# Kernel tuning notes

Measured on AMD Instinct MI355X. Metric: run time of the kernel, lower is better.

The kernel has to match this reference:

```python
import jax, jax.numpy as jnp
import numpy as np

D_MODEL = 4096
NUM_EXPERTS = 64
TOP_K = 2


def setup_inputs() -> dict:
    key = jax.random.key(0)
    kx, kw, kb = jax.random.split(key, 3)
    x = jax.random.normal(kx, (4, 4096, D_MODEL), dtype=jnp.float32)
    # nn.Linear(d_model, num_experts): weight [E, D], bias [E]
    bound = 1.0 / np.sqrt(D_MODEL)
    W = jax.random.uniform(kw, (NUM_EXPERTS, D_MODEL), dtype=jnp.float32, minval=-bound, maxval=bound)
    b = jax.random.uniform(kb, (NUM_EXPERTS,), dtype=jnp.float32, minval=-bound, maxval=bound)
    return {"x": x, "W": W, "b": b}


def reference(x, W, b):
    # logits = gate(x): [B, S, E]
    logits = jnp.einsum("bsd,ed->bse", x, W) + b
    scores = jax.nn.softmax(logits, axis=-1)
    topk_scores, topk_idx = jax.lax.top_k(scores, TOP_K)  # [B,S,K]
    # scatter top-k scores back into a dense [B,S,E] dispatch mask
    onehot = jax.nn.one_hot(topk_idx, NUM_EXPERTS, dtype=scores.dtype)  # [B,S,K,E]
    dispatch_mask = jnp.einsum("bske,bsk->bse", onehot, topk_scores)
    return dispatch_mask
```

## Files before the change

kernel.cpp:

```cpp
#include <hip/hip_runtime.h>
#include <hip/hip_bf16.h>
#include <math.h>
#include <stdint.h>

#define DM 4096
#define NEXP 64
#define BK 64
#define NCH (DM / BK)
#define TOKPB 16

typedef short bf16x8 __attribute__((ext_vector_type(8)));
typedef float f32x4  __attribute__((ext_vector_type(4)));

#define SMEM_BYTES 8192

__device__ __forceinline__ void split2(float f0, float f1, uint32_t& hw, uint32_t& lw) {
    float2 ff; ff.x = f0; ff.y = f1;
    __hip_bfloat162 h = __float22bfloat162_rn(ff);
    union { __hip_bfloat162 b; uint32_t u; } ch; ch.b = h;
    hw = ch.u;
    float h0 = __bfloat162float(h.x);
    float h1 = __bfloat162float(h.y);
    float2 gg; gg.x = f0 - h0; gg.y = f1 - h1;
    __hip_bfloat162 l = __float22bfloat162_rn(gg);
    union { __hip_bfloat162 b; uint32_t u; } cl; cl.b = l;
    lw = cl.u;
}

__global__ __launch_bounds__(512) void wsplit_kernel(const float* __restrict__ W,
                                                     char* __restrict__ blob) {
    const int c   = blockIdx.x;
    const int tid = threadIdx.x;
    const int e   = tid >> 3;
    const int g   = tid & 7;

    const float* src = W + (size_t)e * DM + c * BK + g * 8;
    float x[8];
    *(float4*)(x)     = *(const float4*)(src);
    *(float4*)(x + 4) = *(const float4*)(src + 4);

    uint32_t hiw[4], low[4];
#pragma unroll
    for (int j = 0; j < 4; ++j) split2(x[2 * j], x[2 * j + 1], hiw[j], low[j]);

    const int ks = g >> 2;
    const int ln = (e & 15) | ((g & 3) << 4);
    const int n4 = e >> 4;
    const size_t base = (size_t)c * 16384 + (size_t)ks * 4096 + (size_t)n4 * 1024 + (size_t)ln * 16;
    *(uint4*)(blob + base)        = *(uint4*)hiw;
    *(uint4*)(blob + base + 8192) = *(uint4*)low;
}

__global__ __launch_bounds__(128) void router_mfma_kernel(
    const float* __restrict__ X,
    const char* __restrict__ blob,
    const float* __restrict__ Bv,
    float* __restrict__ out)
{
    __shared__ __align__(16) char smem[SMEM_BYTES];

    const int tid  = threadIdx.x;
    const int lane = tid & 63;
    const int wv   = tid >> 6;
    const long tok0 = (long)blockIdx.x * TOKPB;

    const int tkn = tid >> 3;
    const int kq  = tid & 7;
    const size_t rowbase = (size_t)(tok0 + tkn) * DM + kq * 8;

    f32x4 acc[2];
    acc[0] = (f32x4)0.0f;
    acc[1] = (f32x4)0.0f;

    float xa[8], xb[8];

    auto loadX = [&](float* xr, int c) {
        const float* p = X + rowbase + c * BK;
        *(float4*)(xr)     = *(const float4*)(p);
        *(float4*)(xr + 4) = *(const float4*)(p + 4);
    };

    auto cvtWrite = [&](const float* xr, int buf) {
        uint32_t hw[4], lw[4];
#pragma unroll
        for (int j = 0; j < 4; ++j) split2(xr[2 * j], xr[2 * j + 1], hw[j], lw[j]);
        const int slot = (kq ^ (tkn & 7)) * 16;
        char* bh = smem + ((buf * 2 + 0) * TOKPB + tkn) * 128;
        char* bl = smem + ((buf * 2 + 1) * TOKPB + tkn) * 128;
        *(uint4*)(bh + slot) = *(uint4*)hw;
        *(uint4*)(bl + slot) = *(uint4*)lw;
    };

    const int tk = lane & 15;
    const int kg = lane >> 4;
    const int sw = tk & 7;

    auto compute = [&](int buf, int c) {
        const char* bb = blob + (size_t)c * 16384;
#pragma unroll
        for (int ks = 0; ks < 2; ++ks) {
            const int gA   = ks * 4 + kg;
            const int slot = (gA ^ sw) * 16;
            bf16x8 ah = *(const bf16x8*)(smem + ((buf * 2 + 0) * TOKPB + tk) * 128 + slot);
            bf16x8 al = *(const bf16x8*)(smem + ((buf * 2 + 1) * TOKPB + tk) * 128 + slot);
#pragma unroll
            for (int n = 0; n < 2; ++n) {
                const int n4 = wv * 2 + n;
                const size_t bo = (size_t)ks * 4096 + (size_t)n4 * 1024 + (size_t)lane * 16;
                bf16x8 bh = *(const bf16x8*)(bb + bo);
                bf16x8 bl = *(const bf16x8*)(bb + 8192 + bo);
                acc[n] = __builtin_amdgcn_mfma_f32_16x16x32_bf16(ah, bh, acc[n], 0, 0, 0);
                acc[n] = __builtin_amdgcn_mfma_f32_16x16x32_bf16(ah, bl, acc[n], 0, 0, 0);
                acc[n] = __builtin_amdgcn_mfma_f32_16x16x32_bf16(al, bh, acc[n], 0, 0, 0);
                acc[n] = __builtin_amdgcn_mfma_f32_16x16x32_bf16(al, bl, acc[n], 0, 0, 0);
            }
        }
    };

    loadX(xa, 0);
    cvtWrite(xa, 0);
    __syncthreads();

#pragma unroll 1
    for (int cc = 0; cc < NCH / 2; ++cc) {
        const int c0 = 2 * cc;
        loadX(xb, c0 + 1);
        compute(0, c0);
        cvtWrite(xb, 1);
        __syncthreads();
        if (cc + 1 < NCH / 2) {
            loadX(xa, c0 + 2);
            compute(1, c0 + 1);
            cvtWrite(xa, 0);
        } else {
            compute(1, c0 + 1);
        }
        __syncthreads();
    }

#pragma unroll
    for (int n = 0; n < 2; ++n) {
        const int ee = (wv * 2 + n) * 16 + tk;
#pragma unroll
        for (int r = 0; r < 4; ++r) {
            const int tl = kg * 4 + r;
            *(float*)(smem + tl * 264 + ee * 4) = acc[n][r];
        }
    }
    __syncthreads();

    const float bias = Bv[lane];
#pragma unroll 1
    for (int j = 0; j < 8; ++j) {
        const int t = wv * 8 + j;
        float v = *(const float*)(smem + t * 264 + lane * 4) + bias;

        float m1 = v;        int i1 = lane;
        float m2 = -3.4e38f; int i2 = 127;
#pragma unroll
        for (int s = 1; s < 64; s <<= 1) {
            float om1 = __shfl_xor(m1, s, 64);
            int   oi1 = __shfl_xor(i1, s, 64);
            float om2 = __shfl_xor(m2, s, 64);
            int   oi2 = __shfl_xor(i2, s, 64);
            bool bw = (om1 > m1) || (om1 == m1 && oi1 < i1);
            float l1v = bw ? m1 : om1;  int l1i = bw ? i1 : oi1;
            float w2v = bw ? om2 : m2;  int w2i = bw ? oi2 : i2;
            if (bw) { m1 = om1; i1 = oi1; }
            bool tw = (l1v > w2v) || (l1v == w2v && l1i < w2i);
            m2 = tw ? l1v : w2v;  i2 = tw ? l1i : w2i;
        }

        float p = expf(v - m1);
        float ssum = p;
#pragma unroll
        for (int s = 1; s < 64; s <<= 1) ssum += __shfl_xor(ssum, s, 64);

        float sc = (lane == i1 || lane == i2) ? (p / ssum) : 0.0f;
        out[(size_t)(tok0 + t) * NEXP + lane] = sc;
    }
}

extern "C" void kernel_launch(void* const* d_in, const int* in_sizes, int n_in,
                              void* d_out, int out_size, void* d_ws, size_t ws_size,
                              hipStream_t stream) {
    const float* X  = (const float*)d_in[0];
    const float* W  = (const float*)d_in[1];
    const float* Bv = (const float*)d_in[2];
    float* out = (float*)d_out;

    char* blob = (char*)d_ws;
    wsplit_kernel<<<dim3(NCH), dim3(512), 0, stream>>>(W, blob);

    const int n_tokens = 4 * 4096;
    router_mfma_kernel<<<dim3(n_tokens / TOKPB), dim3(128), 0, stream>>>(X, blob, Bv, out);
}
```

Before: 83.98 us.

## Double tokens per block and split experts across four waves with deeper X prefetch

Each block now handles 32 tokens with 256 threads. Each wave owns 16 experts and runs two 16-token MFMA tiles, so every weight fragment loaded from global memory is reused across both tiles instead of being reloaded per wave. The X loads are also issued one extra chunk ahead to deepen the software pipeline. The costs are a larger shared-memory footprint, more live registers for the prefetch buffers, and half as many blocks in the grid.

```diff
diff --git a/kernel.cpp b/kernel.cpp
--- a/kernel.cpp
+++ b/kernel.cpp
@@ -7,12 +7,12 @@
 #define NEXP 64
 #define BK 64
 #define NCH (DM / BK)
-#define TOKPB 16
+#define TOKPB 32
 
 typedef short bf16x8 __attribute__((ext_vector_type(8)));
 typedef float f32x4  __attribute__((ext_vector_type(4)));
 
-#define SMEM_BYTES 8192
+#define SMEM_BYTES 16384
 
 __device__ __forceinline__ void split2(float f0, float f1, uint32_t& hw, uint32_t& lw) {
     float2 ff; ff.x = f0; ff.y = f1;
@@ -51,7 +51,7 @@
     *(uint4*)(blob + base + 8192) = *(uint4*)low;
 }
 
-__global__ __launch_bounds__(128) void router_mfma_kernel(
+__global__ __launch_bounds__(256) void router_mfma_kernel(
     const float* __restrict__ X,
     const char* __restrict__ blob,
     const float* __restrict__ Bv,
@@ -93,58 +93,54 @@
 
     const int tk = lane & 15;
     const int kg = lane >> 4;
-    const int sw = tk & 7;
+    const int sw = lane & 7;
 
     auto compute = [&](int buf, int c) {
         const char* bb = blob + (size_t)c * 16384;
 #pragma unroll
         for (int ks = 0; ks < 2; ++ks) {
-            const int gA   = ks * 4 + kg;
-            const int slot = (gA ^ sw) * 16;
-            bf16x8 ah = *(const bf16x8*)(smem + ((buf * 2 + 0) * TOKPB + tk) * 128 + slot);
-            bf16x8 al = *(const bf16x8*)(smem + ((buf * 2 + 1) * TOKPB + tk) * 128 + slot);
+            const int slot = ((ks * 4 + kg) ^ sw) * 16;
+            const size_t bo = (size_t)ks * 4096 + (size_t)wv * 1024 + (size_t)lane * 16;
+            bf16x8 bh = *(const bf16x8*)(bb + bo);
+            bf16x8 bl = *(const bf16x8*)(bb + 8192 + bo);
 #pragma unroll
-            for (int n = 0; n < 2; ++n) {
-                const int n4 = wv * 2 + n;
-                const size_t bo = (size_t)ks * 4096 + (size_t)n4 * 1024 + (size_t)lane * 16;
-                bf16x8 bh = *(const bf16x8*)(bb + bo);
-                bf16x8 bl = *(const bf16x8*)(bb + 8192 + bo);
-                acc[n] = __builtin_amdgcn_mfma_f32_16x16x32_bf16(ah, bh, acc[n], 0, 0, 0);
-                acc[n] = __builtin_amdgcn_mfma_f32_16x16x32_bf16(ah, bl, acc[n], 0, 0, 0);
-                acc[n] = __builtin_amdgcn_mfma_f32_16x16x32_bf16(al, bh, acc[n], 0, 0, 0);
-                acc[n] = __builtin_amdgcn_mfma_f32_16x16x32_bf16(al, bl, acc[n], 0, 0, 0);
+            for (int m = 0; m < 2; ++m) {
+                const int row = m * 16 + tk;
+                bf16x8 ah = *(const bf16x8*)(smem + ((buf * 2 + 0) * TOKPB + row) * 128 + slot);
+                bf16x8 al = *(const bf16x8*)(smem + ((buf * 2 + 1) * TOKPB + row) * 128 + slot);
+                acc[m] = __builtin_amdgcn_mfma_f32_16x16x32_bf16(ah, bh, acc[m], 0, 0, 0);
+                acc[m] = __builtin_amdgcn_mfma_f32_16x16x32_bf16(ah, bl, acc[m], 0, 0, 0);
+                acc[m] = __builtin_amdgcn_mfma_f32_16x16x32_bf16(al, bh, acc[m], 0, 0, 0);
+                acc[m] = __builtin_amdgcn_mfma_f32_16x16x32_bf16(al, bl, acc[m], 0, 0, 0);
             }
         }
     };
 
     loadX(xa, 0);
+    loadX(xb, 1);
     cvtWrite(xa, 0);
     __syncthreads();
 
 #pragma unroll 1
     for (int cc = 0; cc < NCH / 2; ++cc) {
         const int c0 = 2 * cc;
-        loadX(xb, c0 + 1);
+        if (c0 + 2 < NCH) loadX(xa, c0 + 2);
         compute(0, c0);
         cvtWrite(xb, 1);
         __syncthreads();
-        if (cc + 1 < NCH / 2) {
-            loadX(xa, c0 + 2);
-            compute(1, c0 + 1);
-            cvtWrite(xa, 0);
-        } else {
-            compute(1, c0 + 1);
-        }
+        if (c0 + 3 < NCH) loadX(xb, c0 + 3);
+        compute(1, c0 + 1);
+        if (c0 + 2 < NCH) cvtWrite(xa, 0);
         __syncthreads();
     }
 
 #pragma unroll
-    for (int n = 0; n < 2; ++n) {
-        const int ee = (wv * 2 + n) * 16 + tk;
+    for (int m = 0; m < 2; ++m) {
+        const int ee = wv * 16 + tk;
 #pragma unroll
         for (int r = 0; r < 4; ++r) {
-            const int tl = kg * 4 + r;
-            *(float*)(smem + tl * 264 + ee * 4) = acc[n][r];
+            const int tl = m * 16 + kg * 4 + r;
+            *(float*)(smem + tl * 264 + ee * 4) = acc[m][r];
         }
     }
     __syncthreads();
@@ -193,5 +189,5 @@
     wsplit_kernel<<<dim3(NCH), dim3(512), 0, stream>>>(W, blob);
 
     const int n_tokens = 4 * 4096;
-    router_mfma_kernel<<<dim3(n_tokens / TOKPB), dim3(128), 0, stream>>>(X, blob, Bv, out);
+    router_mfma_kernel<<<dim3(n_tokens / TOKPB), dim3(256), 0, stream>>>(X, blob, Bv, out);
 }
```

After: 112.9 us. +34.5%, slower.
